# Performance work log

Hardware: AMD Instinct MI355X
Metric: run time of the kernel (lower is better)

## Reference

```python
import jax, jax.numpy as jnp
import numpy as np

B = 8192
D = 128
N_CLASSES = 100
TEMPERATURE = 0.1


def setup_inputs() -> dict:
    key = jax.random.key(0)
    k1, k2 = jax.random.split(key)
    feats = jax.random.normal(k1, (B, D), dtype=jnp.float32)
    # L2-normalise as the docstring assumes
    feats = feats / jnp.linalg.norm(feats, axis=1, keepdims=True)
    labels = jax.random.randint(k2, (B,), 0, N_CLASSES, dtype=jnp.int64)
    return {"features": feats, "labels": labels}


def reference(features, labels):
    features = features.astype(jnp.float32)
    b = features.shape[0]
    sim = (features @ features.T) / TEMPERATURE            # (B, B)
    labels_eq = labels[None, :] == labels[:, None]          # (B, B)
    self_mask = ~jnp.eye(b, dtype=bool)                     # (B, B), False on diag
    pos_mask = labels_eq & self_mask

    sim_max = jax.lax.stop_gradient(jnp.max(sim, axis=1, keepdims=True))
    logits = sim - sim_max                                  # (B, B)
    exp_logits = jnp.exp(logits) * self_mask.astype(jnp.float32)
    log_sum_exp = jnp.log(jnp.sum(exp_logits, axis=1, keepdims=True) + 1e-12)
    log_prob = logits - log_sum_exp                         # (B, B)

    n_positives = jnp.sum(pos_mask.astype(jnp.float32), axis=1)  # (B,)
    valid = n_positives > 0
    mean_log_prob = jnp.sum(pos_mask.astype(jnp.float32) * log_prob, axis=1) \
        / jnp.maximum(n_positives, 1.0)

    valid_f = valid.astype(jnp.float32)
    n_valid = jnp.sum(valid_f)
    loss = -jnp.sum(mean_log_prob * valid_f) / jnp.maximum(n_valid, 1.0)
    # match torch: return 0 if no anchor has a positive
    return jnp.where(n_valid > 0, loss, jnp.float32(0.0))
```

## Files before the change

kernel.cpp:

```cpp
#include <hip/hip_runtime.h>
#include <hip/hip_bf16.h>


#define BB 8192
#define DD 128
#define NC 8
#define COLCHUNK (BB / NC)
#define ITERS (COLCHUNK / 128)
#define TEMP_INV 10.0f
#define MSHIFT 10.5f

typedef __bf16 bf16x8 __attribute__((ext_vector_type(8)));
typedef float floatx4 __attribute__((ext_vector_type(4)));

__device__ inline unsigned short f2bf(float f) {
    unsigned u = __float_as_uint(f);
    return (unsigned short)((u + 0x7FFFu + ((u >> 16) & 1u)) >> 16);
}

__global__ void supcon_detect(const unsigned short* __restrict__ feats_raw,
                              const int* __restrict__ labels_raw,
                              int* __restrict__ flags)
{
    int lane = threadIdx.x;
    unsigned ue = ((unsigned)feats_raw[2 * lane]) << 16;
    float fe = __uint_as_float(ue);
    float ve = fe * fe;
    int odd_or = labels_raw[2 * lane + 1];
#pragma unroll
    for (int m = 1; m < 64; m <<= 1) {
        ve += __shfl_xor(ve, m, 64);
        odd_or |= __shfl_xor(odd_or, m, 64);
    }
    if (lane == 0) {
        bool feats_bf16 = (ve > 0.05f) && (ve < 4.0f);
        flags[0] = feats_bf16 ? 0 : 1;
        flags[1] = (odd_or == 0) ? 1 : 0;
    }
}

__global__ __launch_bounds__(256) void supcon_convert(
    const void* __restrict__ fin, const void* __restrict__ lin,
    const int* __restrict__ flags,
    unsigned short* __restrict__ fbf, int* __restrict__ lab)
{
    int gid = blockIdx.x * 256 + threadIdx.x;
    if (flags[0]) {
        float4 v = ((const float4*)fin)[gid];
        ushort4 o;
        o.x = f2bf(v.x); o.y = f2bf(v.y); o.z = f2bf(v.z); o.w = f2bf(v.w);
        ((ushort4*)fbf)[gid] = o;
    } else {
        ((ushort4*)fbf)[gid] = ((const ushort4*)fin)[gid];
    }
    if (blockIdx.x < 32) {
        int li = blockIdx.x * 256 + threadIdx.x;
        const int* L = (const int*)lin;
        lab[li] = flags[1] ? L[2 * li] : L[li];
    }
}

__global__ __launch_bounds__(256, 2) void supcon_main(
    const unsigned short* __restrict__ Fb, const int* __restrict__ labels,
    float* __restrict__ e_part, float* __restrict__ p_part,
    float* __restrict__ n_part)
{
    __shared__ unsigned char ldsbuf[32768];
    __shared__ float red[3][128][2];

    const int tid  = threadIdx.x;
    const int lane = tid & 63;
    const int wid  = tid >> 6;
    const int wrow = wid >> 1;
    const int wcol = wid & 1;
    const int quad = lane >> 4;
    const int l16  = lane & 15;

    const int chunk   = blockIdx.x;
    const int rowbase = blockIdx.y * 128;
    const int colchunkbase = chunk * COLCHUNK;

    {
        const unsigned char* gA = (const unsigned char*)(Fb) + (size_t)rowbase * 256;
#pragma unroll
        for (int rnd = 0; rnd < 8; ++rnd) {
            int off = rnd * 4096 + tid * 16;
            int row = off >> 8;
            int g   = (off >> 4) & 15;
            int gs  = g ^ (row & 15);
            int4 v  = *(const int4*)(gA + off);
            *(int4*)(&ldsbuf[row * 256 + gs * 16]) = v;
        }
    }
    __syncthreads();

    bf16x8 afrag[4][4];
#pragma unroll
    for (int ti = 0; ti < 4; ++ti) {
        int row = wrow * 64 + ti * 16 + l16;
#pragma unroll
        for (int k = 0; k < 4; ++k) {
            int g  = k * 4 + quad;
            int gs = g ^ (row & 15);
            afrag[ti][k] = *(const bf16x8*)(&ldsbuf[row * 256 + gs * 16]);
        }
    }

    int lab_row[16];
#pragma unroll
    for (int ti = 0; ti < 4; ++ti)
#pragma unroll
        for (int r = 0; r < 4; ++r)
            lab_row[ti * 4 + r] = labels[rowbase + wrow * 64 + ti * 16 + quad * 4 + r];

    float e_acc[16], p_acc[16], n_acc[16];
#pragma unroll
    for (int i = 0; i < 16; ++i) { e_acc[i] = 0.0f; p_acc[i] = 0.0f; n_acc[i] = 0.0f; }

    __syncthreads();

    for (int it = 0; it < ITERS; ++it) {
        int colbase = colchunkbase + it * 128;
        const unsigned char* gB = (const unsigned char*)(Fb) + (size_t)colbase * 256;
#pragma unroll
        for (int rnd = 0; rnd < 8; ++rnd) {
            int off = rnd * 4096 + tid * 16;
            int row = off >> 8;
            int g   = (off >> 4) & 15;
            int gs  = g ^ (row & 15);
            int4 v  = *(const int4*)(gB + off);
            *(int4*)(&ldsbuf[row * 256 + gs * 16]) = v;
        }
        __syncthreads();

#pragma unroll
        for (int tj = 0; tj < 4; ++tj) {
            int coll = wcol * 64 + tj * 16 + l16;
            bf16x8 bfrag[4];
#pragma unroll
            for (int k = 0; k < 4; ++k) {
                int g  = k * 4 + quad;
                int gs = g ^ (coll & 15);
                bfrag[k] = *(const bf16x8*)(&ldsbuf[coll * 256 + gs * 16]);
            }
            floatx4 acc[4];
#pragma unroll
            for (int ti = 0; ti < 4; ++ti) acc[ti] = (floatx4){0.f, 0.f, 0.f, 0.f};
#pragma unroll
            for (int k = 0; k < 4; ++k)
#pragma unroll
                for (int ti = 0; ti < 4; ++ti)
                    acc[ti] = __builtin_amdgcn_mfma_f32_16x16x32_bf16(
                        afrag[ti][k], bfrag[k], acc[ti], 0, 0, 0);

            int col   = colbase + coll;
            int lab_c = labels[col];
#pragma unroll
            for (int ti = 0; ti < 4; ++ti) {
                int row0 = rowbase + wrow * 64 + ti * 16 + quad * 4;
#pragma unroll
                for (int r = 0; r < 4; ++r) {
                    float s = acc[ti][r] * TEMP_INV;
                    int row = row0 + r;
                    bool nd  = (row != col);
                    float ex = __expf(s - MSHIFT);
                    bool pos = nd && (lab_c == lab_row[ti * 4 + r]);
                    e_acc[ti * 4 + r] += nd ? ex : 0.0f;
                    p_acc[ti * 4 + r] += pos ? s : 0.0f;
                    n_acc[ti * 4 + r] += pos ? 1.0f : 0.0f;
                }
            }
        }
        __syncthreads();
    }

#pragma unroll
    for (int i = 0; i < 16; ++i) {
        float e = e_acc[i], p = p_acc[i], n = n_acc[i];
#pragma unroll
        for (int m = 1; m < 16; m <<= 1) {
            e += __shfl_xor(e, m, 64);
            p += __shfl_xor(p, m, 64);
            n += __shfl_xor(n, m, 64);
        }
        if (l16 == 0) {
            int row_local = wrow * 64 + (i >> 2) * 16 + quad * 4 + (i & 3);
            red[0][row_local][wcol] = e;
            red[1][row_local][wcol] = p;
            red[2][row_local][wcol] = n;
        }
    }
    __syncthreads();

    if (tid < 128) {
        size_t idx = (size_t)chunk * BB + (rowbase + tid);
        e_part[idx] = red[0][tid][0] + red[0][tid][1];
        p_part[idx] = red[1][tid][0] + red[1][tid][1];
        n_part[idx] = red[2][tid][0] + red[2][tid][1];
    }
}

__global__ __launch_bounds__(256) void supcon_reduce(
    const float* __restrict__ e_part, const float* __restrict__ p_part,
    const float* __restrict__ n_part, float* __restrict__ partials)
{
    int row = blockIdx.x * 256 + threadIdx.x;
    float e = 0.f, p = 0.f, n = 0.f;
#pragma unroll
    for (int c = 0; c < NC; ++c) {
        size_t idx = (size_t)c * BB + row;
        e += e_part[idx]; p += p_part[idx]; n += n_part[idx];
    }
    float contrib = 0.f, vld = 0.f;
    if (n > 0.5f) {
        vld = 1.0f;
        contrib = -(p / n - MSHIFT - logf(e));
    }
#pragma unroll
    for (int m = 1; m < 64; m <<= 1) {
        contrib += __shfl_xor(contrib, m, 64);
        vld     += __shfl_xor(vld, m, 64);
    }
    __shared__ float rl[4], rv[4];
    int lane = threadIdx.x & 63, w = threadIdx.x >> 6;
    if (lane == 0) { rl[w] = contrib; rv[w] = vld; }
    __syncthreads();
    if (threadIdx.x == 0) {
        partials[blockIdx.x * 2]     = rl[0] + rl[1] + rl[2] + rl[3];
        partials[blockIdx.x * 2 + 1] = rv[0] + rv[1] + rv[2] + rv[3];
    }
}

__global__ void supcon_final(const float* __restrict__ partials, float* __restrict__ out)
{
    int lane = threadIdx.x;
    float L = (lane < 32) ? partials[lane * 2]     : 0.0f;
    float V = (lane < 32) ? partials[lane * 2 + 1] : 0.0f;
#pragma unroll
    for (int m = 1; m < 64; m <<= 1) {
        L += __shfl_xor(L, m, 64);
        V += __shfl_xor(V, m, 64);
    }
    if (lane == 0) out[0] = (V > 0.5f) ? (L / V) : 0.0f;
}

extern "C" void kernel_launch(void* const* d_in, const int* in_sizes, int n_in,
                              void* d_out, int out_size, void* d_ws, size_t ws_size,
                              hipStream_t stream)
{
    const void* Fin = d_in[0];
    const void* Lin = d_in[1];

    unsigned short* fbf = (unsigned short*)d_ws;
    int*   lab      = (int*)((char*)d_ws + (size_t)BB * DD * 2);
    float* e_part   = (float*)((char*)lab + (size_t)BB * 4);
    float* p_part   = e_part + (size_t)NC * BB;
    float* n_part   = p_part + (size_t)NC * BB;
    float* partials = n_part + (size_t)NC * BB;
    int*   flags    = (int*)(partials + 64);

    supcon_detect<<<1, 64, 0, stream>>>((const unsigned short*)Fin, (const int*)Lin, flags);
    supcon_convert<<<(BB * DD / 4 + 255) / 256, 256, 0, stream>>>(Fin, Lin, flags, fbf, lab);

    dim3 grid(NC, BB / 128);
    supcon_main<<<grid, 256, 0, stream>>>(fbf, lab, e_part, p_part, n_part);
    supcon_reduce<<<32, 256, 0, stream>>>(e_part, p_part, n_part, partials);
    supcon_final<<<1, 64, 0, stream>>>(partials, (float*)d_out);
}
```

Baseline: 106.7 us.

## Fuse detect/final kernels, drop diagonal masking, use exp2 epilogue, raise occupancy

Merges the type-detection kernel into the convert kernel and replaces the final reduction kernel with atomics and a last-block-done counter, removing two launches. The inner epilogue drops the per-element diagonal and positive masks: the diagonal dot products are saved separately and subtracted in the reduce step. Scale and shift are folded into a single FMA feeding a native exp2. Column chunks double to 16 and launch bounds target 4 blocks per SM for more parallelism. The trade-offs are slightly different rounding from subtracting the self term and reliance on atomic ordering for the final result.

```diff
diff --git a/kernel.cpp b/kernel.cpp
--- a/kernel.cpp
+++ b/kernel.cpp
@@ -4,48 +4,50 @@
 
 #define BB 8192
 #define DD 128
-#define NC 8
+#define NC 16
 #define COLCHUNK (BB / NC)
 #define ITERS (COLCHUNK / 128)
 #define TEMP_INV 10.0f
 #define MSHIFT 10.5f
+#define C1F 14.426950408889634f
+#define C2F -15.148297929334116f
 
 typedef __bf16 bf16x8 __attribute__((ext_vector_type(8)));
 typedef float floatx4 __attribute__((ext_vector_type(4)));
+
+__device__ inline float fast_exp2(float x) {
+#if __has_builtin(__builtin_amdgcn_exp2f)
+    return __builtin_amdgcn_exp2f(x);
+#else
+    return exp2f(x);
+#endif
+}
 
 __device__ inline unsigned short f2bf(float f) {
     unsigned u = __float_as_uint(f);
     return (unsigned short)((u + 0x7FFFu + ((u >> 16) & 1u)) >> 16);
 }
 
-__global__ void supcon_detect(const unsigned short* __restrict__ feats_raw,
-                              const int* __restrict__ labels_raw,
-                              int* __restrict__ flags)
-{
-    int lane = threadIdx.x;
-    unsigned ue = ((unsigned)feats_raw[2 * lane]) << 16;
+__global__ __launch_bounds__(256) void supcon_convert(
+    const void* __restrict__ fin, const void* __restrict__ lin,
+    unsigned short* __restrict__ fbf, int* __restrict__ lab,
+    float* __restrict__ accbuf)
+{
+    int lane = threadIdx.x & 63;
+    unsigned ue = ((unsigned)((const unsigned short*)fin)[2 * lane]) << 16;
     float fe = __uint_as_float(ue);
     float ve = fe * fe;
-    int odd_or = labels_raw[2 * lane + 1];
+    int odd_or = ((const int*)lin)[2 * lane + 1];
 #pragma unroll
     for (int m = 1; m < 64; m <<= 1) {
         ve += __shfl_xor(ve, m, 64);
         odd_or |= __shfl_xor(odd_or, m, 64);
     }
-    if (lane == 0) {
-        bool feats_bf16 = (ve > 0.05f) && (ve < 4.0f);
-        flags[0] = feats_bf16 ? 0 : 1;
-        flags[1] = (odd_or == 0) ? 1 : 0;
-    }
-}
-
-__global__ __launch_bounds__(256) void supcon_convert(
-    const void* __restrict__ fin, const void* __restrict__ lin,
-    const int* __restrict__ flags,
-    unsigned short* __restrict__ fbf, int* __restrict__ lab)
-{
+    bool f_bf16 = (ve > 0.05f) && (ve < 4.0f);
+    bool l_i64  = (odd_or == 0);
+
     int gid = blockIdx.x * 256 + threadIdx.x;
-    if (flags[0]) {
+    if (!f_bf16) {
         float4 v = ((const float4*)fin)[gid];
         ushort4 o;
         o.x = f2bf(v.x); o.y = f2bf(v.y); o.z = f2bf(v.z); o.w = f2bf(v.w);
@@ -56,14 +58,19 @@
     if (blockIdx.x < 32) {
         int li = blockIdx.x * 256 + threadIdx.x;
         const int* L = (const int*)lin;
-        lab[li] = flags[1] ? L[2 * li] : L[li];
-    }
-}
-
-__global__ __launch_bounds__(256, 2) void supcon_main(
+        lab[li] = l_i64 ? L[2 * li] : L[li];
+    }
+    if (blockIdx.x == 0 && threadIdx.x == 0) {
+        accbuf[0] = 0.0f;
+        accbuf[1] = 0.0f;
+        ((unsigned*)accbuf)[2] = 0u;
+    }
+}
+
+__global__ __launch_bounds__(256, 4) void supcon_main(
     const unsigned short* __restrict__ Fb, const int* __restrict__ labels,
     float* __restrict__ e_part, float* __restrict__ p_part,
-    float* __restrict__ n_part)
+    float* __restrict__ n_part, float* __restrict__ diag)
 {
     __shared__ unsigned char ldsbuf[32768];
     __shared__ float red[3][128][2];
@@ -153,21 +160,34 @@
                     acc[ti] = __builtin_amdgcn_mfma_f32_16x16x32_bf16(
                         afrag[ti][k], bfrag[k], acc[ti], 0, 0, 0);
 
-            int col   = colbase + coll;
-            int lab_c = labels[col];
+            {
+                int ctb = colbase + wcol * 64 + tj * 16;
+                unsigned u = (unsigned)(ctb - (rowbase + wrow * 64));
+                if (u < 64u) {
+#pragma unroll
+                    for (int ti2 = 0; ti2 < 4; ++ti2) {
+                        if (u == (unsigned)(ti2 * 16)) {
+#pragma unroll
+                            for (int r = 0; r < 4; ++r)
+                                if (l16 == quad * 4 + r)
+                                    diag[ctb + l16] = acc[ti2][r];
+                        }
+                    }
+                }
+            }
+
+            int lab_c = labels[colbase + coll];
 #pragma unroll
             for (int ti = 0; ti < 4; ++ti) {
-                int row0 = rowbase + wrow * 64 + ti * 16 + quad * 4;
 #pragma unroll
                 for (int r = 0; r < 4; ++r) {
-                    float s = acc[ti][r] * TEMP_INV;
-                    int row = row0 + r;
-                    bool nd  = (row != col);
-                    float ex = __expf(s - MSHIFT);
-                    bool pos = nd && (lab_c == lab_row[ti * 4 + r]);
-                    e_acc[ti * 4 + r] += nd ? ex : 0.0f;
-                    p_acc[ti * 4 + r] += pos ? s : 0.0f;
-                    n_acc[ti * 4 + r] += pos ? 1.0f : 0.0f;
+                    int i = ti * 4 + r;
+                    float a  = acc[ti][r];
+                    float ex = fast_exp2(__builtin_fmaf(a, C1F, C2F));
+                    e_acc[i] += ex;
+                    float peq = (lab_c == lab_row[i]) ? 1.0f : 0.0f;
+                    p_acc[i] = __builtin_fmaf(peq, a, p_acc[i]);
+                    n_acc[i] += peq;
                 }
             }
         }
@@ -202,7 +222,8 @@
 
 __global__ __launch_bounds__(256) void supcon_reduce(
     const float* __restrict__ e_part, const float* __restrict__ p_part,
-    const float* __restrict__ n_part, float* __restrict__ partials)
+    const float* __restrict__ n_part, const float* __restrict__ diag,
+    float* __restrict__ accbuf, float* __restrict__ out)
 {
     int row = blockIdx.x * 256 + threadIdx.x;
     float e = 0.f, p = 0.f, n = 0.f;
@@ -211,10 +232,15 @@
         size_t idx = (size_t)c * BB + row;
         e += e_part[idx]; p += p_part[idx]; n += n_part[idx];
     }
+    float d = diag[row];
+    e -= fast_exp2(__builtin_fmaf(d, C1F, C2F));
+    p -= d;
+    n -= 1.0f;
+
     float contrib = 0.f, vld = 0.f;
     if (n > 0.5f) {
         vld = 1.0f;
-        contrib = -(p / n - MSHIFT - logf(e));
+        contrib = -(p * TEMP_INV / n - MSHIFT - logf(e));
     }
 #pragma unroll
     for (int m = 1; m < 64; m <<= 1) {
@@ -226,22 +252,18 @@
     if (lane == 0) { rl[w] = contrib; rv[w] = vld; }
     __syncthreads();
     if (threadIdx.x == 0) {
-        partials[blockIdx.x * 2]     = rl[0] + rl[1] + rl[2] + rl[3];
-        partials[blockIdx.x * 2 + 1] = rv[0] + rv[1] + rv[2] + rv[3];
-    }
-}
-
-__global__ void supcon_final(const float* __restrict__ partials, float* __restrict__ out)
-{
-    int lane = threadIdx.x;
-    float L = (lane < 32) ? partials[lane * 2]     : 0.0f;
-    float V = (lane < 32) ? partials[lane * 2 + 1] : 0.0f;
-#pragma unroll
-    for (int m = 1; m < 64; m <<= 1) {
-        L += __shfl_xor(L, m, 64);
-        V += __shfl_xor(V, m, 64);
-    }
-    if (lane == 0) out[0] = (V > 0.5f) ? (L / V) : 0.0f;
+        float L = rl[0] + rl[1] + rl[2] + rl[3];
+        float V = rv[0] + rv[1] + rv[2] + rv[3];
+        atomicAdd(&accbuf[0], L);
+        atomicAdd(&accbuf[1], V);
+        __threadfence();
+        unsigned t = atomicAdd((unsigned*)accbuf + 2, 1u);
+        if (t == 31u) {
+            float Ls = atomicAdd(&accbuf[0], 0.0f);
+            float Vs = atomicAdd(&accbuf[1], 0.0f);
+            out[0] = (Vs > 0.5f) ? (Ls / Vs) : 0.0f;
+        }
+    }
 }
 
 extern "C" void kernel_launch(void* const* d_in, const int* in_sizes, int n_in,
@@ -256,14 +278,13 @@
     float* e_part   = (float*)((char*)lab + (size_t)BB * 4);
     float* p_part   = e_part + (size_t)NC * BB;
     float* n_part   = p_part + (size_t)NC * BB;
-    float* partials = n_part + (size_t)NC * BB;
-    int*   flags    = (int*)(partials + 64);
-
-    supcon_detect<<<1, 64, 0, stream>>>((const unsigned short*)Fin, (const int*)Lin, flags);
-    supcon_convert<<<(BB * DD / 4 + 255) / 256, 256, 0, stream>>>(Fin, Lin, flags, fbf, lab);
+    float* diag     = n_part + (size_t)NC * BB;
+    float* accbuf   = diag + BB;
+
+    supcon_convert<<<BB * DD / 4 / 256, 256, 0, stream>>>(Fin, Lin, fbf, lab, accbuf);
 
     dim3 grid(NC, BB / 128);
-    supcon_main<<<grid, 256, 0, stream>>>(fbf, lab, e_part, p_part, n_part);
-    supcon_reduce<<<32, 256, 0, stream>>>(e_part, p_part, n_part, partials);
-    supcon_final<<<1, 64, 0, stream>>>(partials, (float*)d_out);
-}
+    supcon_main<<<grid, 256, 0, stream>>>(fbf, lab, e_part, p_part, n_part, diag);
+
+    supcon_reduce<<<32, 256, 0, stream>>>(e_part, p_part, n_part, diag, accbuf, (float*)d_out);
+}
```

New measurement: 267.5 us. 2.51x slower.
